# Optimization experiments

Hardware: AMD Instinct MI355X
Metric: run time of the kernel (lower is better)

## Reference

```python
import jax, jax.numpy as jnp
import numpy as np
import math

B, T = 16, 60
N_CLASSES = 80
N_ANCHORS = 3
N_CH = 5 + N_CLASSES
STRIDES = (8, 16, 32)
IMG = 608
ANCHORS = np.array([[12,16],[19,36],[40,28],[36,75],[76,55],[72,146],[142,110],[192,243],[459,401]], dtype=np.float32)
IGNORE_THRE = 0.5


def _clip_log(x):
    # torch F.binary_cross_entropy clamps log at -100
    return jnp.maximum(jnp.log(x), -100.0)


def _bce_sum(p, t, w=None):
    l = -(t * _clip_log(p) + (1.0 - t) * _clip_log(1.0 - p))
    if w is not None:
        l = l * w
    return jnp.sum(l)


def _ciou_wh(wh_a, wh_b):
    # truth boxes are xyxy [0,0,w,h]; wh_a [B,T,2], wh_b [9,2] -> CIoU [B,T,9]
    wa = wh_a[..., 0:1]; ha = wh_a[..., 1:2]
    wb = wh_b[:, 0];     hb = wh_b[:, 1]
    iw = jnp.minimum(wa, wb); ih = jnp.minimum(ha, hb)
    en = ((iw > 0) & (ih > 0)).astype(wh_a.dtype)
    area_i = iw * ih * en
    area_u = wa * ha + wb * hb - area_i
    iou = area_i / area_u
    c2 = jnp.maximum(wa, wb) ** 2 + jnp.maximum(ha, hb) ** 2 + 1e-16
    rho2 = ((wa - wb) ** 2 + (ha - hb) ** 2) / 4.0
    v = (4.0 / math.pi ** 2) * (jnp.arctan(wa / ha) - jnp.arctan(wb / hb)) ** 2
    alpha = v / (1.0 - iou + v)
    return iou - (rho2 / c2 + v * alpha)


def _iou_xywh(pred, truth):
    # pred [B,N,4] (cx,cy,w,h), truth [B,T,4] -> IoU [B,N,T]
    p_xy = pred[:, :, None, :2]; p_wh = pred[:, :, None, 2:]
    t_xy = truth[:, None, :, :2]; t_wh = truth[:, None, :, 2:]
    tl = jnp.maximum(p_xy - p_wh * 0.5, t_xy - t_wh * 0.5)
    br = jnp.minimum(p_xy + p_wh * 0.5, t_xy + t_wh * 0.5)
    en = jnp.all(tl < br, axis=-1).astype(pred.dtype)
    area_i = jnp.prod(br - tl, axis=-1) * en
    area_p = pred[..., 2] * pred[..., 3]
    area_t = truth[..., 2] * truth[..., 3]
    return area_i / (area_p[:, :, None] + area_t[:, None, :] - area_i)


def _level_losses(x, labels, oid):
    dt = x.dtype
    stride = STRIDES[oid]
    fsize = IMG // stride
    Bsz = x.shape[0]
    out = x.reshape(Bsz, N_ANCHORS, N_CH, fsize, fsize).transpose(0, 1, 3, 4, 2)  # [B,A,F,F,C]
    sig = jax.nn.sigmoid(out)
    sxy, raw_wh, sobj, scls = sig[..., :2], out[..., 2:4], sig[..., 4], sig[..., 5:]

    all_anch = jnp.asarray(ANCHORS / stride, dt)           # [9,2] grid units
    masked_anch = all_anch[3 * oid: 3 * oid + 3]           # [3,2]
    g = jnp.arange(fsize, dtype=dt)
    px = sxy[..., 0] + g[None, None, None, :]
    py = sxy[..., 1] + g[None, None, :, None]
    pw = jnp.exp(raw_wh[..., 0]) * masked_anch[:, 0][None, :, None, None]
    ph = jnp.exp(raw_wh[..., 1]) * masked_anch[:, 1][None, :, None, None]
    pred = jnp.stack([px, py, pw, ph], axis=-1)            # [B,A,F,F,4]

    lab = jax.lax.stop_gradient(labels.astype(dt))         # targets carry no grad (as in torch)
    valid = jnp.sum(lab, axis=-1) > 0                      # [B,T]
    tx = (lab[..., 2] + lab[..., 0]) / (stride * 2.0)
    ty = (lab[..., 3] + lab[..., 1]) / (stride * 2.0)
    tw = (lab[..., 2] - lab[..., 0]) / stride
    th = (lab[..., 3] - lab[..., 1]) / stride
    ii = jnp.clip(tx.astype(jnp.int32), 0, fsize - 1)      # int16 trunc in torch, coords >= 0
    jj = jnp.clip(ty.astype(jnp.int32), 0, fsize - 1)

    ciou = _ciou_wh(jnp.stack([tw, th], -1), all_anch)     # [B,T,9]
    ciou = jnp.where(valid[..., None], ciou, -1e9)
    best_all = jnp.argmax(ciou, axis=-1)                   # [B,T]
    best_n = best_all % 3
    best_mask = (best_all // 3 == oid) & valid             # anchor owned by this level
    has_match = jnp.any(best_mask, axis=1)                 # [B]; torch `continue` if none

    truth_box = jnp.stack([tx, ty, tw, th], -1) * valid[..., None].astype(dt)
    ious = _iou_xywh(jax.lax.stop_gradient(pred).reshape(Bsz, -1, 4), truth_box)
    ious = jnp.where(valid[:, None, :], ious, 0.0)
    ignore = (jnp.max(ious, axis=-1) > IGNORE_THRE).reshape(Bsz, N_ANCHORS, fsize, fsize)
    obj_mask = jnp.where(has_match[:, None, None, None], 1.0 - ignore.astype(dt), jnp.asarray(1.0, dt))

    # scatter positive assignments; dummy batch row Bsz absorbs masked-out writes
    bidx = jnp.where(best_mask, jnp.arange(Bsz, dtype=jnp.int32)[:, None], Bsz)
    pad1 = lambda a: jnp.concatenate([a, jnp.zeros((1,) + a.shape[1:], a.dtype)], 0)
    obj_mask = pad1(obj_mask).at[bidx, best_n, jj, ii].set(1.0)[:Bsz]
    tgt_mask = jnp.zeros((Bsz + 1, N_ANCHORS, fsize, fsize, 4 + N_CLASSES), dt).at[bidx, best_n, jj, ii].set(1.0)[:Bsz]
    scale = jnp.sqrt(2.0 - tw * th / float(fsize * fsize))  # [B,T]
    tgt_scale = jnp.zeros((Bsz + 1, N_ANCHORS, fsize, fsize, 2), dt).at[bidx, best_n, jj, ii].set(
        jnp.broadcast_to(scale[..., None], scale.shape + (2,)))[:Bsz]
    aw = masked_anch[best_n, 0]; ah = masked_anch[best_n, 1]
    vec = jnp.concatenate([
        (tx - jnp.trunc(tx))[..., None],
        (ty - jnp.trunc(ty))[..., None],
        jnp.log(tw / aw + 1e-16)[..., None],
        jnp.log(th / ah + 1e-16)[..., None],
        jnp.ones_like(tx)[..., None],
        jax.nn.one_hot(lab[..., 4].astype(jnp.int32), N_CLASSES, dtype=dt),
    ], axis=-1)                                            # [B,T,N_CH]
    target = jnp.zeros((Bsz + 1, N_ANCHORS, fsize, fsize, N_CH), dt).at[bidx, best_n, jj, ii].set(vec)[:Bsz]

    o_xy = sxy * tgt_mask[..., :2]
    o_wh = raw_wh * tgt_mask[..., 2:4] * tgt_scale
    o_obj = sobj * obj_mask
    o_cls = scls * tgt_mask[..., 4:]
    t_xy = target[..., :2] * tgt_mask[..., :2]
    t_wh = target[..., 2:4] * tgt_mask[..., 2:4] * tgt_scale
    t_obj = target[..., 4] * obj_mask
    t_cls = target[..., 5:] * tgt_mask[..., 4:]

    l_xy = _bce_sum(o_xy, t_xy, tgt_scale * tgt_scale)
    l_wh = 0.5 * jnp.sum((o_wh - t_wh) ** 2)
    l_obj = _bce_sum(o_obj, t_obj)
    l_cls = _bce_sum(o_cls, t_cls)
    l_l2 = (jnp.sum((o_xy - t_xy) ** 2) + jnp.sum((o_wh - t_wh) ** 2)
            + jnp.sum((o_obj - t_obj) ** 2) + jnp.sum((o_cls - t_cls) ** 2))
    return l_xy, l_wh, l_obj, l_cls, l_l2


def setup_inputs() -> dict:
    key = jax.random.key(0)
    ks = jax.random.split(key, 8)
    x0 = jax.random.normal(ks[0], (B, N_ANCHORS * N_CH, 76, 76), jnp.float32)
    x1 = jax.random.normal(ks[1], (B, N_ANCHORS * N_CH, 38, 38), jnp.float32)
    x2 = jax.random.normal(ks[2], (B, N_ANCHORS * N_CH, 19, 19), jnp.float32)
    cx = jax.random.uniform(ks[3], (B, T), minval=70.0, maxval=538.0)
    cy = jax.random.uniform(ks[4], (B, T), minval=70.0, maxval=538.0)
    bw = jax.random.uniform(ks[5], (B, T), minval=8.0, maxval=128.0)
    bh = jax.random.uniform(ks[6], (B, T), minval=8.0, maxval=128.0)
    cls = jax.random.randint(ks[7], (B, T), 0, N_CLASSES).astype(jnp.float32)
    labels = jnp.stack([cx - bw / 2, cy - bh / 2, cx + bw / 2, cy + bh / 2, cls], axis=-1)
    nvalid = jax.random.randint(jax.random.fold_in(key, 99), (B,), 5, T + 1)
    mask = (jnp.arange(T)[None, :] < nvalid[:, None]).astype(jnp.float32)
    labels = labels * mask[..., None]  # zero padding rows (nlabel = rows with sum>0)
    return {"x0": x0, "x1": x1, "x2": x2, "labels": labels}


def reference(x0, x1, x2, labels):
    totals = [jnp.asarray(0.0, x0.dtype)] * 5
    for oid, x in enumerate((x0, x1, x2)):
        parts = _level_losses(x, labels, oid)
        totals = [a + b for a, b in zip(totals, parts)]
    l_xy, l_wh, l_obj, l_cls, l_l2 = totals
    loss = l_xy + l_wh + l_obj + l_cls
    return loss, l_xy, l_wh, l_obj, l_cls, l_l2
```

## Files before the change

kernel.cpp:

```cpp
#include <hip/hip_runtime.h>

#define BATCH 16
#define TT 60
#define NCLS 80
#define NB0 68
#define NB1 17
#define NB2 5
#define NBX (NB0 + NB1 + NB2)
#define NBLK (NBX * BATCH)

__constant__ float c_aw[9] = {12.f,19.f,40.f,36.f,76.f,72.f,142.f,192.f,459.f};
__constant__ float c_ah[9] = {16.f,36.f,28.f,75.f,55.f,146.f,110.f,243.f,401.f};

__device__ __forceinline__ float sigf(float x){ return 1.0f/(1.0f+expf(-x)); }
__device__ __forceinline__ float clogf_(float x){ return fmaxf(logf(x), -100.0f); }
__device__ __forceinline__ float bcef(float p, float t){
    return -(t*clogf_(p) + (1.0f-t)*clogf_(1.0f-p));
}

__global__ __launch_bounds__(256) void main_kernel(
    const float* __restrict__ x0, const float* __restrict__ x1,
    const float* __restrict__ x2, const float* __restrict__ labels,
    float* __restrict__ ws)
{
    const int bx = blockIdx.x, b = blockIdx.y, tid = threadIdx.x;
    int lvl, lb, fs;
    const float* x;
    if (bx < NB0)            { lvl = 0; lb = bx;             x = x0; fs = 76; }
    else if (bx < NB0 + NB1) { lvl = 1; lb = bx - NB0;       x = x1; fs = 38; }
    else                     { lvl = 2; lb = bx - NB0 - NB1; x = x2; fs = 19; }
    const float invs = 1.0f/(float)(8 << lvl);
    const int fs2 = fs*fs;
    const int ncell = 3*fs2;
    const int lin = lb*256 + tid;

    __shared__ float  s_atan[9];
    __shared__ float4 s_box[TT];
    __shared__ int    s_mcell[TT], s_mcls[TT];
    __shared__ float  s_vx[TT], s_vy[TT], s_vw[TT], s_vh[TT], s_sc[TT];
    __shared__ int    s_nv, s_nm;

    float l0=0,l1=0,l2=0,l3=0,l4=0;
    if (tid < TT) {
        const float* lab = labels + ((size_t)b*TT + tid)*5;
        l0=lab[0]; l1=lab[1]; l2=lab[2]; l3=lab[3]; l4=lab[4];
    }
    if (tid < 9) s_atan[tid] = atanf(c_aw[tid]/c_ah[tid]);

    float v0=0,v1=0,v2=0,v3=0,v4=0;
    int a=0, rem=0, ci=0, cj=0;
    if (lin < ncell) {
        a = lin/fs2; rem = lin - a*fs2; cj = rem/fs; ci = rem - cj*fs;
        const float* xb = x + ((size_t)b*255 + a*85)*(size_t)fs2 + rem;
        v0 = xb[0]; v1 = xb[(size_t)fs2]; v2 = xb[(size_t)2*fs2];
        v3 = xb[(size_t)3*fs2]; v4 = xb[(size_t)4*fs2];
    }

    if (tid < 64) {
        bool valid=false, best=false;
        float tx=0,ty=0,tw=0,th=0;
        int best_all=0;
        if (tid < TT) {
            valid = ((((l0+l1)+l2)+l3)+l4) > 0.0f;
            tx = (l2+l0)*(0.5f*invs);
            ty = (l3+l1)*(0.5f*invs);
            tw = (l2-l0)*invs;
            th = (l3-l1)*invs;
            if (valid) {
                float ta = atanf(tw/th);
                float twth = tw*th;
                float bestv = 0.0f;
                for (int k=0;k<9;k++){
                    float wb=c_aw[k]*invs, hb=c_ah[k]*invs;
                    float iw=fminf(tw,wb), ih=fminf(th,hb);
                    float en=(iw>0.f && ih>0.f)?1.f:0.f;
                    float ai=iw*ih*en;
                    float au=twth+wb*hb-ai;
                    float iou=ai/au;
                    float mw=fmaxf(tw,wb), mh=fmaxf(th,hb);
                    float c2=mw*mw+mh*mh+1e-16f;
                    float rho2=((tw-wb)*(tw-wb)+(th-hb)*(th-hb))*0.25f;
                    float da=ta-s_atan[k];
                    float v=0.40528473456935109f*da*da;
                    float alpha=v/((1.f-iou)+v);
                    float cv=iou-(rho2/c2+v*alpha);
                    if (k==0 || cv>bestv){ bestv=cv; best_all=k; }
                }
            }
        }
        int bn = best_all % 3;
        best = valid && ((best_all/3) == lvl);
        unsigned long long vm = __ballot(valid);
        unsigned long long bm = __ballot(best);
        unsigned long long below = (tid==0) ? 0ULL : ((1ULL<<tid)-1ULL);
        if (valid){
            int r = __popcll(vm & below);
            s_box[r] = make_float4(tx-0.5f*tw, ty-0.5f*th, tx+0.5f*tw, ty+0.5f*th);
        }
        if (best){
            int r = __popcll(bm & below);
            int ti=(int)tx, tj=(int)ty;
            int ii = ti<0?0:(ti>fs-1?fs-1:ti);
            int jj = tj<0?0:(tj>fs-1?fs-1:tj);
            s_mcell[r] = (bn*fs+jj)*fs+ii;
            s_mcls[r]  = (int)l4;
            s_sc[r]    = sqrtf(2.f - tw*th/(float)(fs*fs));
            s_vx[r]    = tx - truncf(tx);
            s_vy[r]    = ty - truncf(ty);
            float aw = c_aw[3*lvl+bn]*invs, ah = c_ah[3*lvl+bn]*invs;
            s_vw[r]    = logf(tw/aw + 1e-16f);
            s_vh[r]    = logf(th/ah + 1e-16f);
        }
        if (tid==0){ s_nv = __popcll(vm); s_nm = __popcll(bm); }
    }
    __syncthreads();

    const int nv = s_nv, nm = s_nm;
    float lxy=0.f, lwh=0.f, lobj=0.f, lcls=0.f, ll2=0.f;
    int mt = -1;
    int qoff = 0, qcls = 0;
    if (lin < ncell) {
        const float sx = sigf(v0), sy = sigf(v1), sobj = sigf(v4);
        const float aw = c_aw[3*lvl+a]*invs, ah = c_ah[3*lvl+a]*invs;
        const float px = sx + (float)ci;
        const float py = sy + (float)cj;
        const float pw = expf(v2)*aw;
        const float ph = expf(v3)*ah;
        const float ap = pw*ph;

        for (int k=0;k<nm;k++){
            if (s_mcell[k] == lin) mt = k;
        }

        bool ign = false;
        if (nm > 0 && mt < 0) {
            const float xl = px-0.5f*pw, xr = px+0.5f*pw;
            const float yl = py-0.5f*ph, yr = py+0.5f*ph;
            #pragma unroll 4
            for (int t=0;t<nv;t++){
                float4 tb = s_box[t];
                float at2 = (tb.z-tb.x)*(tb.w-tb.y);
                float w = fmaxf(fminf(xr,tb.z) - fmaxf(xl,tb.x), 0.f);
                float h = fmaxf(fminf(yr,tb.w) - fmaxf(yl,tb.y), 0.f);
                ign = ign || (3.f*(w*h) > ap+at2);
            }
        }
        float om = (nm>0) ? (ign ? 0.f : 1.f) : 1.f;
        float t4 = 0.f;
        if (mt >= 0){ om = 1.f; t4 = 1.f; }
        const float oo = sobj*om, to = t4*om;
        lobj = bcef(oo, to);
        const float d = oo - to;
        ll2 = d*d;
        if (mt >= 0) {
            const float sc = s_sc[mt], w2 = sc*sc;
            const float mvx = s_vx[mt], mvy = s_vy[mt];
            lxy = w2*(bcef(sx,mvx) + bcef(sy,mvy));
            const float dx = sx-mvx, dy = sy-mvy;
            const float dw = sc*(v2 - s_vw[mt]);
            const float dh = sc*(v3 - s_vh[mt]);
            lwh = 0.5f*(dw*dw + dh*dh);
            ll2 += dx*dx + dy*dy + dw*dw + dh*dh;
            qoff = (a*85+5)*fs2 + rem;
            qcls = s_mcls[mt];
        }
    }

    const int ln = tid & 63;
    const size_t bbase = (size_t)b*255*(size_t)fs2;
    unsigned long long mb = __ballot(mt >= 0);
    while (mb) {
        int src = __ffsll(mb) - 1; mb &= mb - 1;
        int qo = __shfl(qoff, src), cc = __shfl(qcls, src);
        const size_t base = bbase + (size_t)qo;
        float p = sigf(x[base + (size_t)ln*fs2]);
        float tt = (ln==cc) ? 1.f : 0.f;
        lcls += bcef(p, tt);
        float dd = p - tt; ll2 += dd*dd;
        if (ln < NCLS-64) {
            int c = 64+ln;
            p = sigf(x[base + (size_t)c*fs2]);
            tt = (c==cc) ? 1.f : 0.f;
            lcls += bcef(p, tt);
            dd = p - tt; ll2 += dd*dd;
        }
    }

    for (int off=32; off>0; off>>=1){
        lxy  += __shfl_down(lxy,  off);
        lwh  += __shfl_down(lwh,  off);
        lobj += __shfl_down(lobj, off);
        lcls += __shfl_down(lcls, off);
        ll2  += __shfl_down(ll2,  off);
    }
    __shared__ float red[4][5];
    const int wid = tid >> 6;
    if (ln == 0){ red[wid][0]=lxy; red[wid][1]=lwh; red[wid][2]=lobj; red[wid][3]=lcls; red[wid][4]=ll2; }
    __syncthreads();
    if (tid == 0){
        const int blk = b*NBX + bx;
        ws[0*NBLK + blk] = red[0][0]+red[1][0]+red[2][0]+red[3][0];
        ws[1*NBLK + blk] = red[0][1]+red[1][1]+red[2][1]+red[3][1];
        ws[2*NBLK + blk] = red[0][2]+red[1][2]+red[2][2]+red[3][2];
        ws[3*NBLK + blk] = red[0][3]+red[1][3]+red[2][3]+red[3][3];
        ws[4*NBLK + blk] = red[0][4]+red[1][4]+red[2][4]+red[3][4];
    }
}

__global__ __launch_bounds__(256) void fin_kernel(const float* __restrict__ ws, float* __restrict__ out){
    const int tid = threadIdx.x;
    float s[5] = {0.f,0.f,0.f,0.f,0.f};
    for (int i = tid; i < NBLK; i += 256){
        #pragma unroll
        for (int c=0;c<5;c++) s[c] += ws[c*NBLK + i];
    }
    for (int off=32; off>0; off>>=1){
        #pragma unroll
        for (int c=0;c<5;c++) s[c] += __shfl_down(s[c], off);
    }
    __shared__ float red[4][5];
    const int wid = tid >> 6, ln = tid & 63;
    if (ln == 0){ for (int c=0;c<5;c++) red[wid][c] = s[c]; }
    __syncthreads();
    if (tid == 0){
        float t_xy  = red[0][0]+red[1][0]+red[2][0]+red[3][0];
        float t_wh  = red[0][1]+red[1][1]+red[2][1]+red[3][1];
        float t_obj = red[0][2]+red[1][2]+red[2][2]+red[3][2];
        float t_cls = red[0][3]+red[1][3]+red[2][3]+red[3][3];
        float t_l2  = red[0][4]+red[1][4]+red[2][4]+red[3][4];
        out[0] = t_xy + t_wh + t_obj + t_cls;
        out[1] = t_xy; out[2] = t_wh; out[3] = t_obj; out[4] = t_cls; out[5] = t_l2;
    }
}

extern "C" void kernel_launch(void* const* d_in, const int* in_sizes, int n_in,
                              void* d_out, int out_size, void* d_ws, size_t ws_size,
                              hipStream_t stream) {
    const float* x0 = (const float*)d_in[0];
    const float* x1 = (const float*)d_in[1];
    const float* x2 = (const float*)d_in[2];
    const float* labels = (const float*)d_in[3];
    float* out = (float*)d_out;
    float* ws = (float*)d_ws;

    main_kernel<<<dim3(NBX, BATCH), 256, 0, stream>>>(x0, x1, x2, labels, ws);
    fin_kernel<<<1, 256, 0, stream>>>(ws, out);
}
```

Measured before the change: 27.58 us.

## Process four cells per thread to amortize per-block label setup

Each thread now handles four grid cells instead of one, which cuts the block count by about four. The per-block label preprocessing (anchor matching, atan and the shared-memory setup) is therefore repeated far less often. Each shared-memory truth box load is also reused across four predictions in the ignore-IoU loop. In exchange each thread uses more registers, there are fewer blocks to spread across the GPU's compute units, and the level-2 tail blocks carry more idle lanes.

```diff
diff --git a/kernel.cpp b/kernel.cpp
--- a/kernel.cpp
+++ b/kernel.cpp
@@ -3,9 +3,11 @@
 #define BATCH 16
 #define TT 60
 #define NCLS 80
-#define NB0 68
-#define NB1 17
-#define NB2 5
+#define NC 4
+#define CPB (256*NC)
+#define NB0 17
+#define NB1 5
+#define NB2 2
 #define NBX (NB0 + NB1 + NB2)
 #define NBLK (NBX * BATCH)
 
@@ -32,7 +34,6 @@
     const float invs = 1.0f/(float)(8 << lvl);
     const int fs2 = fs*fs;
     const int ncell = 3*fs2;
-    const int lin = lb*256 + tid;
 
     __shared__ float  s_atan[9];
     __shared__ float4 s_box[TT];
@@ -47,13 +48,22 @@
     }
     if (tid < 9) s_atan[tid] = atanf(c_aw[tid]/c_ah[tid]);
 
-    float v0=0,v1=0,v2=0,v3=0,v4=0;
-    int a=0, rem=0, ci=0, cj=0;
-    if (lin < ncell) {
-        a = lin/fs2; rem = lin - a*fs2; cj = rem/fs; ci = rem - cj*fs;
-        const float* xb = x + ((size_t)b*255 + a*85)*(size_t)fs2 + rem;
-        v0 = xb[0]; v1 = xb[(size_t)fs2]; v2 = xb[(size_t)2*fs2];
-        v3 = xb[(size_t)3*fs2]; v4 = xb[(size_t)4*fs2];
+    int   lin[NC], aa[NC], rem[NC], ci[NC], cj[NC];
+    bool  cc[NC];
+    float v0[NC], v1[NC], v2[NC], v3[NC], v4[NC];
+    #pragma unroll
+    for (int q=0;q<NC;q++){
+        lin[q] = lb*CPB + q*256 + tid;
+        cc[q]  = lin[q] < ncell;
+        aa[q]=0; rem[q]=0; ci[q]=0; cj[q]=0;
+        v0[q]=0; v1[q]=0; v2[q]=0; v3[q]=0; v4[q]=0;
+        if (cc[q]) {
+            aa[q] = lin[q]/fs2; rem[q] = lin[q] - aa[q]*fs2;
+            cj[q] = rem[q]/fs;  ci[q]  = rem[q] - cj[q]*fs;
+            const float* xb = x + ((size_t)b*255 + aa[q]*85)*(size_t)fs2 + rem[q];
+            v0[q] = xb[0]; v1[q] = xb[(size_t)fs2]; v2[q] = xb[(size_t)2*fs2];
+            v3[q] = xb[(size_t)3*fs2]; v4[q] = xb[(size_t)4*fs2];
+        }
     }
 
     if (tid < 64) {
@@ -117,72 +127,88 @@
 
     const int nv = s_nv, nm = s_nm;
     float lxy=0.f, lwh=0.f, lobj=0.f, lcls=0.f, ll2=0.f;
-    int mt = -1;
-    int qoff = 0, qcls = 0;
-    if (lin < ncell) {
-        const float sx = sigf(v0), sy = sigf(v1), sobj = sigf(v4);
-        const float aw = c_aw[3*lvl+a]*invs, ah = c_ah[3*lvl+a]*invs;
-        const float px = sx + (float)ci;
-        const float py = sy + (float)cj;
-        const float pw = expf(v2)*aw;
-        const float ph = expf(v3)*ah;
-        const float ap = pw*ph;
-
-        for (int k=0;k<nm;k++){
-            if (s_mcell[k] == lin) mt = k;
-        }
-
-        bool ign = false;
-        if (nm > 0 && mt < 0) {
-            const float xl = px-0.5f*pw, xr = px+0.5f*pw;
-            const float yl = py-0.5f*ph, yr = py+0.5f*ph;
-            #pragma unroll 4
-            for (int t=0;t<nv;t++){
-                float4 tb = s_box[t];
-                float at2 = (tb.z-tb.x)*(tb.w-tb.y);
-                float w = fmaxf(fminf(xr,tb.z) - fmaxf(xl,tb.x), 0.f);
-                float h = fmaxf(fminf(yr,tb.w) - fmaxf(yl,tb.y), 0.f);
-                ign = ign || (3.f*(w*h) > ap+at2);
+    int   mt[NC];
+    int   qoff[NC], qcls[NC];
+    float sx[NC], sy[NC], so[NC], pxl[NC], pxr[NC], pyl[NC], pyr[NC], ap[NC];
+    bool  ign[NC];
+    #pragma unroll
+    for (int q=0;q<NC;q++){
+        mt[q] = -1; qoff[q] = 0; qcls[q] = 0; ign[q] = false;
+        sx[q] = sigf(v0[q]); sy[q] = sigf(v1[q]); so[q] = sigf(v4[q]);
+        const float aw = c_aw[3*lvl+aa[q]]*invs, ah = c_ah[3*lvl+aa[q]]*invs;
+        const float px = sx[q] + (float)ci[q];
+        const float py = sy[q] + (float)cj[q];
+        const float pw = expf(v2[q])*aw;
+        const float ph = expf(v3[q])*ah;
+        ap[q]  = pw*ph;
+        pxl[q] = px-0.5f*pw; pxr[q] = px+0.5f*pw;
+        pyl[q] = py-0.5f*ph; pyr[q] = py+0.5f*ph;
+    }
+
+    for (int k=0;k<nm;k++){
+        int mc = s_mcell[k];
+        #pragma unroll
+        for (int q=0;q<NC;q++) if (mc == lin[q]) mt[q] = k;
+    }
+
+    if (nm > 0) {
+        #pragma unroll 4
+        for (int t=0;t<nv;t++){
+            float4 tb = s_box[t];
+            float at2 = (tb.z-tb.x)*(tb.w-tb.y);
+            #pragma unroll
+            for (int q=0;q<NC;q++){
+                float w = fmaxf(fminf(pxr[q],tb.z) - fmaxf(pxl[q],tb.x), 0.f);
+                float h = fmaxf(fminf(pyr[q],tb.w) - fmaxf(pyl[q],tb.y), 0.f);
+                ign[q] = ign[q] || (3.f*(w*h) > ap[q]+at2);
             }
         }
-        float om = (nm>0) ? (ign ? 0.f : 1.f) : 1.f;
+    }
+
+    #pragma unroll
+    for (int q=0;q<NC;q++){
+        if (!cc[q]) continue;
+        float om = (nm>0) ? (ign[q] ? 0.f : 1.f) : 1.f;
         float t4 = 0.f;
-        if (mt >= 0){ om = 1.f; t4 = 1.f; }
-        const float oo = sobj*om, to = t4*om;
-        lobj = bcef(oo, to);
-        const float d = oo - to;
-        ll2 = d*d;
-        if (mt >= 0) {
-            const float sc = s_sc[mt], w2 = sc*sc;
-            const float mvx = s_vx[mt], mvy = s_vy[mt];
-            lxy = w2*(bcef(sx,mvx) + bcef(sy,mvy));
-            const float dx = sx-mvx, dy = sy-mvy;
-            const float dw = sc*(v2 - s_vw[mt]);
-            const float dh = sc*(v3 - s_vh[mt]);
-            lwh = 0.5f*(dw*dw + dh*dh);
+        if (mt[q] >= 0){ om = 1.f; t4 = 1.f; }
+        float oo = so[q]*om, to = t4*om;
+        lobj += bcef(oo, to);
+        float d = oo - to; ll2 += d*d;
+        if (mt[q] >= 0) {
+            const int m = mt[q];
+            float sc = s_sc[m], w2 = sc*sc;
+            float mvx = s_vx[m], mvy = s_vy[m];
+            lxy += w2*(bcef(sx[q],mvx) + bcef(sy[q],mvy));
+            float dx = sx[q]-mvx, dy = sy[q]-mvy;
+            float dw = sc*(v2[q] - s_vw[m]);
+            float dh = sc*(v3[q] - s_vh[m]);
+            lwh += 0.5f*(dw*dw + dh*dh);
             ll2 += dx*dx + dy*dy + dw*dw + dh*dh;
-            qoff = (a*85+5)*fs2 + rem;
-            qcls = s_mcls[mt];
+            qoff[q] = (aa[q]*85+5)*fs2 + rem[q];
+            qcls[q] = s_mcls[m];
         }
     }
 
     const int ln = tid & 63;
     const size_t bbase = (size_t)b*255*(size_t)fs2;
-    unsigned long long mb = __ballot(mt >= 0);
-    while (mb) {
-        int src = __ffsll(mb) - 1; mb &= mb - 1;
-        int qo = __shfl(qoff, src), cc = __shfl(qcls, src);
-        const size_t base = bbase + (size_t)qo;
-        float p = sigf(x[base + (size_t)ln*fs2]);
-        float tt = (ln==cc) ? 1.f : 0.f;
-        lcls += bcef(p, tt);
-        float dd = p - tt; ll2 += dd*dd;
-        if (ln < NCLS-64) {
-            int c = 64+ln;
-            p = sigf(x[base + (size_t)c*fs2]);
-            tt = (c==cc) ? 1.f : 0.f;
+    #pragma unroll
+    for (int q=0;q<NC;q++){
+        unsigned long long mb = __ballot(mt[q] >= 0);
+        while (mb) {
+            int src = __ffsll(mb) - 1; mb &= mb - 1;
+            int qo = __shfl(qoff[q], src), cls = __shfl(qcls[q], src);
+            const size_t base = bbase + (size_t)qo;
+            float p = sigf(x[base + (size_t)ln*fs2]);
+            float tt = (ln==cls) ? 1.f : 0.f;
             lcls += bcef(p, tt);
-            dd = p - tt; ll2 += dd*dd;
+            float dd = p - tt; ll2 += dd*dd;
+            if (ln < NCLS-64) {
+                int c = 64+ln;
+                p = sigf(x[base + (size_t)c*fs2]);
+                tt = (c==cls) ? 1.f : 0.f;
+                lcls += bcef(p, tt);
+                dd = p - tt; ll2 += dd*dd;
+            }
         }
     }
 
```

New measurement: 29.87 us. +8.3%, slower.
